# Performance work log

Hardware: AMD Instinct MI355X
Metric: run time of the kernel (lower is better)

The kernel has to match this reference:

```python
import jax, jax.numpy as jnp
import numpy as np

B, N, C, D = 64, 1024, 128, 64

def setup_inputs() -> dict:
    key = jax.random.key(0)
    ks = jax.random.split(key, 7)
    # kaiming_normal_ on weights (fan_in = C), default zero-ish biases kept as Linear default uniform; use small uniform
    std = float(np.sqrt(2.0 / C))
    bb = float(1.0 / np.sqrt(C))
    return {
        "x": jax.random.normal(ks[0], (B, N, C), jnp.float32),
        "Wq": jax.random.normal(ks[1], (C, D), jnp.float32) * std,
        "bq": jax.random.uniform(ks[2], (D,), jnp.float32, -bb, bb),
        "Wk": jax.random.normal(ks[3], (C, D), jnp.float32) * std,
        "bk": jax.random.uniform(ks[4], (D,), jnp.float32, -bb, bb),
        "Wv": jax.random.normal(ks[5], (C, D), jnp.float32) * std,
        "bv": jax.random.uniform(ks[6], (D,), jnp.float32, -bb, bb),
    }

def reference(x, Wq, bq, Wk, bk, Wv, bv):
    q = jax.nn.relu(jnp.einsum('bnc,cd->bnd', x, Wq) + bq)  # [B,N,D]
    k = jax.nn.relu(jnp.einsum('bnc,cd->bnd', x, Wk) + bk)
    v = jax.nn.relu(jnp.einsum('bnc,cd->bnd', x, Wv) + bv)
    scores = jnp.einsum('bnd,bmd->bnm', q, k) / jnp.sqrt(jnp.asarray(D, q.dtype))
    attn = jax.nn.softmax(scores, axis=-1)
    out = jnp.einsum('bnm,bmd->bnd', attn, v)
    return out + q
```

## Files before the change

### kernel.cpp

```cpp
#include <hip/hip_runtime.h>
#include <hip/hip_bf16.h>


#define Bsz 64
#define Nsz 1024
#define Csz 128
#define Dsz 64

typedef __attribute__((ext_vector_type(8))) short short8;
typedef __attribute__((ext_vector_type(4))) float f32x4;
typedef __attribute__((ext_vector_type(4))) short s16x4;

__device__ __forceinline__ unsigned short f2bf(float f) {
    union { float f; unsigned u; } v; v.f = f;
    unsigned r = v.u + 0x7FFF + ((v.u >> 16) & 1);
    return (unsigned short)(r >> 16);
}
__device__ __forceinline__ float bf2f(unsigned short h) {
    union { unsigned u; float f; } v; v.u = ((unsigned)h) << 16;
    return v.f;
}

__global__ __launch_bounds__(256, 3) void qkv_kernel(
    const float* __restrict__ x,
    const float* __restrict__ Wq, const float* __restrict__ bq,
    const float* __restrict__ Wk, const float* __restrict__ bk,
    const float* __restrict__ Wv, const float* __restrict__ bv,
    float* __restrict__ qf, unsigned short* __restrict__ qs,
    unsigned short* __restrict__ ksc, unsigned short* __restrict__ vt)
{
    __shared__ short xh[8192];
    __shared__ short xl[8192];
    const int t    = threadIdx.x;
    const int lane = t & 63;
    const int l16  = lane & 15, quad = lane >> 4;
    const int dt   = t >> 6;
    const long rowbase = (long)blockIdx.x * 64;

    {
        const int row = t & 63;
        const float* xrow = x + (rowbase + row) * Csz;
        #pragma unroll
        for (int p = 0; p < 4; p++) {
            int cb = (t >> 6) + p * 4;
            float4 a = *(const float4*)(xrow + cb * 8);
            float4 b = *(const float4*)(xrow + cb * 8 + 4);
            float f[8] = {a.x, a.y, a.z, a.w, b.x, b.y, b.z, b.w};
            short8 hi, lo;
            #pragma unroll
            for (int i = 0; i < 8; i++) {
                unsigned short h = f2bf(f[i]);
                hi[i] = (short)h;
                lo[i] = (short)f2bf(f[i] - bf2f(h));
            }
            int unit = ((row >> 4) * 4 + (cb >> 2)) * 64 + ((row & 15) | ((cb & 3) << 4));
            *(short8*)&xh[unit * 8] = hi;
            *(short8*)&xl[unit * 8] = lo;
        }
    }

    short8 wqh[4], wql[4], wkf[4], wvf[4];
    #pragma unroll
    for (int ksi = 0; ksi < 4; ksi++) {
        #pragma unroll
        for (int j = 0; j < 8; j++) {
            int c = ksi * 32 + quad * 8 + j;
            int d = dt * 16 + l16;
            float w = Wq[c * Dsz + d];
            unsigned short h = f2bf(w);
            wqh[ksi][j] = (short)h;
            wql[ksi][j] = (short)f2bf(w - bf2f(h));
            wkf[ksi][j] = (short)f2bf(Wk[c * Dsz + d]);
            wvf[ksi][j] = (short)f2bf(Wv[c * Dsz + d]);
        }
    }
    __syncthreads();

    f32x4 aq[4], akk[4], avv[4];
    #pragma unroll
    for (int i = 0; i < 4; i++) {
        aq[i]  = (f32x4){0.f, 0.f, 0.f, 0.f};
        akk[i] = (f32x4){0.f, 0.f, 0.f, 0.f};
        avv[i] = (f32x4){0.f, 0.f, 0.f, 0.f};
    }

    #pragma unroll
    for (int ksi = 0; ksi < 4; ksi++) {
        #pragma unroll
        for (int rt = 0; rt < 4; rt++) {
            short8 ah = *(const short8*)&xh[((rt * 4 + ksi) * 64 + lane) * 8];
            short8 al = *(const short8*)&xl[((rt * 4 + ksi) * 64 + lane) * 8];
            aq[rt]  = __builtin_amdgcn_mfma_f32_16x16x32_bf16(ah, wqh[ksi], aq[rt], 0, 0, 0);
            aq[rt]  = __builtin_amdgcn_mfma_f32_16x16x32_bf16(al, wqh[ksi], aq[rt], 0, 0, 0);
            aq[rt]  = __builtin_amdgcn_mfma_f32_16x16x32_bf16(ah, wql[ksi], aq[rt], 0, 0, 0);
            akk[rt] = __builtin_amdgcn_mfma_f32_16x16x32_bf16(ah, wkf[ksi], akk[rt], 0, 0, 0);
            avv[rt] = __builtin_amdgcn_mfma_f32_16x16x32_bf16(ah, wvf[ksi], avv[rt], 0, 0, 0);
        }
    }

    const int d = dt * 16 + l16;
    const float bqd = bq[d], bkd = bk[d], bvd = bv[d];
    const long bidx = rowbase >> 10;
    const int nloc = (int)(rowbase & 1023);
    const float SC = 0.125f * 1.44269504f;
    unsigned short* vrow = vt + bidx * (Dsz * Nsz) + (long)d * Nsz + nloc;
    #pragma unroll
    for (int rt = 0; rt < 4; rt++) {
        #pragma unroll
        for (int r = 0; r < 4; r++) {
            long n = rowbase + rt * 16 + quad * 4 + r;
            float q = fmaxf(aq[rt][r]  + bqd, 0.f);
            float k = fmaxf(akk[rt][r] + bkd, 0.f);
            float v = fmaxf(avv[rt][r] + bvd, 0.f);
            qf[n * Dsz + d]  = q;
            qs[n * Dsz + d]  = f2bf(q * SC);
            ksc[n * Dsz + d] = f2bf(k);
            vrow[(quad * 4 + r) * 4 + rt] = f2bf(v);
        }
    }
}

__global__ __launch_bounds__(256) void attn_kernel(
    const unsigned short* __restrict__ qs,
    const unsigned short* __restrict__ ksc,
    const unsigned short* __restrict__ vt,
    const float* __restrict__ qf,
    float* __restrict__ out)
{
    __shared__ short Ks[64][72];
    __shared__ short Vt[64][72];
    __shared__ short Pl[4][16][72];

    const int t    = threadIdx.x;
    const int wave = t >> 6;
    const int lane = t & 63;
    const int l16  = lane & 15;
    const int quad = lane >> 4;
    const int b    = blockIdx.x & 63;
    const int qt   = blockIdx.x >> 6;

    const long qrow = (long)b * Nsz + qt * 64 + wave * 16 + l16;
    const short8 aq0 = *(const short8*)(qs + qrow * Dsz + quad * 8);
    const short8 aq1 = *(const short8*)(qs + qrow * Dsz + 32 + quad * 8);

    f32x4 O[4];
    #pragma unroll
    for (int cb = 0; cb < 4; cb++) O[cb] = (f32x4){0.f, 0.f, 0.f, 0.f};
    float lsum[4] = {0.f, 0.f, 0.f, 0.f};

    const unsigned short* kbatch = ksc + (long)b * Nsz * Dsz;
    const unsigned short* vbatch = vt  + (long)b * Dsz * Nsz;

    for (int kt = 0; kt < 16; kt++) {
        const unsigned short* kg = kbatch + (long)kt * 64 * Dsz;
        #pragma unroll
        for (int p = 0; p < 2; p++) {
            int idx = t + p * 256;
            int key = idx >> 3, dc = (idx & 7) * 8;
            *(short8*)&Ks[key][dc] = *(const short8*)(kg + key * Dsz + dc);
        }
        const unsigned short* vg = vbatch + kt * 64;
        #pragma unroll
        for (int p = 0; p < 2; p++) {
            int idx = t + p * 256;
            int dim = idx >> 3, kc = (idx & 7) * 8;
            *(short8*)&Vt[dim][kc] = *(const short8*)(vg + (long)dim * Nsz + kc);
        }
        __syncthreads();

        f32x4 s[4];
        #pragma unroll
        for (int kb = 0; kb < 4; kb++) {
            short8 b0 = *(const short8*)&Ks[kb * 16 + l16][quad * 8];
            short8 b1 = *(const short8*)&Ks[kb * 16 + l16][32 + quad * 8];
            f32x4 acc = (f32x4){0.f, 0.f, 0.f, 0.f};
            acc = __builtin_amdgcn_mfma_f32_16x16x32_bf16(aq0, b0, acc, 0, 0, 0);
            acc = __builtin_amdgcn_mfma_f32_16x16x32_bf16(aq1, b1, acc, 0, 0, 0);
            s[kb] = acc;
        }

        #pragma unroll
        for (int r = 0; r < 4; r++) {
            float p0 = __builtin_amdgcn_exp2f(s[0][r]);
            float p1 = __builtin_amdgcn_exp2f(s[1][r]);
            float p2 = __builtin_amdgcn_exp2f(s[2][r]);
            float p3 = __builtin_amdgcn_exp2f(s[3][r]);
            lsum[r] += (p0 + p1) + (p2 + p3);
            s16x4 pk = { (short)f2bf(p0), (short)f2bf(p1),
                         (short)f2bf(p2), (short)f2bf(p3) };
            *(s16x4*)&Pl[wave][quad * 4 + r][l16 * 4] = pk;
        }

        #pragma unroll
        for (int ck = 0; ck < 2; ck++) {
            short8 ap = *(const short8*)&Pl[wave][l16][ck * 32 + quad * 8];
            #pragma unroll
            for (int cb = 0; cb < 4; cb++) {
                short8 bv = *(const short8*)&Vt[cb * 16 + l16][ck * 32 + quad * 8];
                O[cb] = __builtin_amdgcn_mfma_f32_16x16x32_bf16(ap, bv, O[cb], 0, 0, 0);
            }
        }
        __syncthreads();
    }

    #pragma unroll
    for (int r = 0; r < 4; r++) {
        #pragma unroll
        for (int off = 1; off < 16; off <<= 1)
            lsum[r] += __shfl_xor(lsum[r], off);
    }

    const long obase = ((long)b * Nsz + qt * 64 + wave * 16) * Dsz;
    #pragma unroll
    for (int r = 0; r < 4; r++) {
        float rl = 1.0f / lsum[r];
        int row = quad * 4 + r;
        #pragma unroll
        for (int cb = 0; cb < 4; cb++) {
            long idx = obase + (long)row * Dsz + cb * 16 + l16;
            out[idx] = O[cb][r] * rl + qf[idx];
        }
    }
}

extern "C" void kernel_launch(void* const* d_in, const int* in_sizes, int n_in,
                              void* d_out, int out_size, void* d_ws, size_t ws_size,
                              hipStream_t stream) {
    const float* x  = (const float*)d_in[0];
    const float* Wq = (const float*)d_in[1];
    const float* bq = (const float*)d_in[2];
    const float* Wk = (const float*)d_in[3];
    const float* bk = (const float*)d_in[4];
    const float* Wv = (const float*)d_in[5];
    const float* bv = (const float*)d_in[6];
    float* out = (float*)d_out;

    char* ws = (char*)d_ws;
    float*          qf  = (float*)ws;
    unsigned short* qsc = (unsigned short*)(ws + 16777216);
    unsigned short* ksc = (unsigned short*)(ws + 25165824);
    unsigned short* vtc = (unsigned short*)(ws + 33554432);

    qkv_kernel<<<dim3(1024), dim3(256), 0, stream>>>(
        x, Wq, bq, Wk, bk, Wv, bv, qf, qsc, ksc, vtc);
    attn_kernel<<<dim3(Bsz * 16), dim3(256), 0, stream>>>(
        qsc, ksc, vtc, qf, out);
}
```

Baseline: 144.0 us.

## Drop fp32 Q buffer, load K/V directly to registers, double query rows per wave

```diff
diff --git a/kernel.cpp b/kernel.cpp
--- a/kernel.cpp
+++ b/kernel.cpp
@@ -9,7 +9,6 @@
 
 typedef __attribute__((ext_vector_type(8))) short short8;
 typedef __attribute__((ext_vector_type(4))) float f32x4;
-typedef __attribute__((ext_vector_type(4))) short s16x4;
 
 __device__ __forceinline__ unsigned short f2bf(float f) {
     union { float f; unsigned u; } v; v.f = f;
@@ -20,14 +19,22 @@
     union { unsigned u; float f; } v; v.u = ((unsigned)h) << 16;
     return v.f;
 }
-
-__global__ __launch_bounds__(256, 3) void qkv_kernel(
+__device__ __forceinline__ unsigned pack_bf16rn(float lo, float hi) {
+    unsigned ulo = __float_as_uint(lo) + 0x8000u;
+    unsigned uhi = __float_as_uint(hi) + 0x8000u;
+    return __builtin_amdgcn_perm(uhi, ulo, 0x07060302u);
+}
+
+#define SCq (0.125f * 1.44269504f)
+#define INV_SC (1.0f / (0.125f * 1.44269504f))
+
+__global__ __launch_bounds__(256, 2) void qkv_kernel(
     const float* __restrict__ x,
     const float* __restrict__ Wq, const float* __restrict__ bq,
     const float* __restrict__ Wk, const float* __restrict__ bk,
     const float* __restrict__ Wv, const float* __restrict__ bv,
-    float* __restrict__ qf, unsigned short* __restrict__ qs,
-    unsigned short* __restrict__ ksc, unsigned short* __restrict__ vt)
+    unsigned short* __restrict__ qs, unsigned short* __restrict__ ksc,
+    unsigned short* __restrict__ vt)
 {
     __shared__ short xh[8192];
     __shared__ short xl[8192];
@@ -35,29 +42,8 @@
     const int lane = t & 63;
     const int l16  = lane & 15, quad = lane >> 4;
     const int dt   = t >> 6;
-    const long rowbase = (long)blockIdx.x * 64;
-
-    {
-        const int row = t & 63;
-        const float* xrow = x + (rowbase + row) * Csz;
-        #pragma unroll
-        for (int p = 0; p < 4; p++) {
-            int cb = (t >> 6) + p * 4;
-            float4 a = *(const float4*)(xrow + cb * 8);
-            float4 b = *(const float4*)(xrow + cb * 8 + 4);
-            float f[8] = {a.x, a.y, a.z, a.w, b.x, b.y, b.z, b.w};
-            short8 hi, lo;
-            #pragma unroll
-            for (int i = 0; i < 8; i++) {
-                unsigned short h = f2bf(f[i]);
-                hi[i] = (short)h;
-                lo[i] = (short)f2bf(f[i] - bf2f(h));
-            }
-            int unit = ((row >> 4) * 4 + (cb >> 2)) * 64 + ((row & 15) | ((cb & 3) << 4));
-            *(short8*)&xh[unit * 8] = hi;
-            *(short8*)&xl[unit * 8] = lo;
-        }
-    }
+    const long rowbase = (long)blockIdx.x * 128;
+    const int d = dt * 16 + l16;
 
     short8 wqh[4], wql[4], wkf[4], wvf[4];
     #pragma unroll
@@ -65,7 +51,6 @@
         #pragma unroll
         for (int j = 0; j < 8; j++) {
             int c = ksi * 32 + quad * 8 + j;
-            int d = dt * 16 + l16;
             float w = Wq[c * Dsz + d];
             unsigned short h = f2bf(w);
             wqh[ksi][j] = (short)h;
@@ -74,62 +59,88 @@
             wvf[ksi][j] = (short)f2bf(Wv[c * Dsz + d]);
         }
     }
-    __syncthreads();
-
-    f32x4 aq[4], akk[4], avv[4];
-    #pragma unroll
-    for (int i = 0; i < 4; i++) {
-        aq[i]  = (f32x4){0.f, 0.f, 0.f, 0.f};
-        akk[i] = (f32x4){0.f, 0.f, 0.f, 0.f};
-        avv[i] = (f32x4){0.f, 0.f, 0.f, 0.f};
-    }
-
-    #pragma unroll
-    for (int ksi = 0; ksi < 4; ksi++) {
+    const float bqd = bq[d], bkd = bk[d], bvd = bv[d];
+    const long b = rowbase >> 10;
+
+    for (int chunk = 0; chunk < 2; chunk++) {
+        const long rowc = rowbase + chunk * 64;
+        if (chunk) __syncthreads();
+
+        {
+            const int row = t & 63;
+            const float* xrow = x + (rowc + row) * Csz;
+            #pragma unroll
+            for (int p = 0; p < 4; p++) {
+                int cb = (t >> 6) + p * 4;
+                float4 a = *(const float4*)(xrow + cb * 8);
+                float4 bb = *(const float4*)(xrow + cb * 8 + 4);
+                float f[8] = {a.x, a.y, a.z, a.w, bb.x, bb.y, bb.z, bb.w};
+                short8 hi, lo;
+                #pragma unroll
+                for (int i = 0; i < 8; i++) {
+                    unsigned short h = f2bf(f[i]);
+                    hi[i] = (short)h;
+                    lo[i] = (short)f2bf(f[i] - bf2f(h));
+                }
+                int unit = ((row >> 4) * 4 + (cb >> 2)) * 64 + ((row & 15) | ((cb & 3) << 4));
+                *(short8*)&xh[unit * 8] = hi;
+                *(short8*)&xl[unit * 8] = lo;
+            }
+        }
+        __syncthreads();
+
+        f32x4 aq[4], ak[4], av[4];
+        #pragma unroll
+        for (int i = 0; i < 4; i++) {
+            aq[i] = (f32x4){0.f, 0.f, 0.f, 0.f};
+            ak[i] = (f32x4){0.f, 0.f, 0.f, 0.f};
+            av[i] = (f32x4){0.f, 0.f, 0.f, 0.f};
+        }
+        #pragma unroll
+        for (int ksi = 0; ksi < 4; ksi++) {
+            #pragma unroll
+            for (int rt = 0; rt < 4; rt++) {
+                short8 ah = *(const short8*)&xh[((rt * 4 + ksi) * 64 + lane) * 8];
+                short8 al = *(const short8*)&xl[((rt * 4 + ksi) * 64 + lane) * 8];
+                aq[rt] = __builtin_amdgcn_mfma_f32_16x16x32_bf16(ah, wqh[ksi], aq[rt], 0, 0, 0);
+                aq[rt] = __builtin_amdgcn_mfma_f32_16x16x32_bf16(al, wqh[ksi], aq[rt], 0, 0, 0);
+                aq[rt] = __builtin_amdgcn_mfma_f32_16x16x32_bf16(ah, wql[ksi], aq[rt], 0, 0, 0);
+                ak[rt] = __builtin_amdgcn_mfma_f32_16x16x32_bf16(ah, wkf[ksi], ak[rt], 0, 0, 0);
+                av[rt] = __builtin_amdgcn_mfma_f32_16x16x32_bf16(ah, wvf[ksi], av[rt], 0, 0, 0);
+            }
+        }
+
+        float vv[16];
         #pragma unroll
         for (int rt = 0; rt < 4; rt++) {
-            short8 ah = *(const short8*)&xh[((rt * 4 + ksi) * 64 + lane) * 8];
-            short8 al = *(const short8*)&xl[((rt * 4 + ksi) * 64 + lane) * 8];
-            aq[rt]  = __builtin_amdgcn_mfma_f32_16x16x32_bf16(ah, wqh[ksi], aq[rt], 0, 0, 0);
-            aq[rt]  = __builtin_amdgcn_mfma_f32_16x16x32_bf16(al, wqh[ksi], aq[rt], 0, 0, 0);
-            aq[rt]  = __builtin_amdgcn_mfma_f32_16x16x32_bf16(ah, wql[ksi], aq[rt], 0, 0, 0);
-            akk[rt] = __builtin_amdgcn_mfma_f32_16x16x32_bf16(ah, wkf[ksi], akk[rt], 0, 0, 0);
-            avv[rt] = __builtin_amdgcn_mfma_f32_16x16x32_bf16(ah, wvf[ksi], avv[rt], 0, 0, 0);
-        }
-    }
-
-    const int d = dt * 16 + l16;
-    const float bqd = bq[d], bkd = bk[d], bvd = bv[d];
-    const long bidx = rowbase >> 10;
-    const int nloc = (int)(rowbase & 1023);
-    const float SC = 0.125f * 1.44269504f;
-    unsigned short* vrow = vt + bidx * (Dsz * Nsz) + (long)d * Nsz + nloc;
-    #pragma unroll
-    for (int rt = 0; rt < 4; rt++) {
-        #pragma unroll
-        for (int r = 0; r < 4; r++) {
-            long n = rowbase + rt * 16 + quad * 4 + r;
-            float q = fmaxf(aq[rt][r]  + bqd, 0.f);
-            float k = fmaxf(akk[rt][r] + bkd, 0.f);
-            float v = fmaxf(avv[rt][r] + bvd, 0.f);
-            qf[n * Dsz + d]  = q;
-            qs[n * Dsz + d]  = f2bf(q * SC);
-            ksc[n * Dsz + d] = f2bf(k);
-            vrow[(quad * 4 + r) * 4 + rt] = f2bf(v);
-        }
-    }
-}
-
-__global__ __launch_bounds__(256) void attn_kernel(
+            #pragma unroll
+            for (int r = 0; r < 4; r++) {
+                long n = rowc + rt * 16 + quad * 4 + r;
+                float q = fmaxf(aq[rt][r] + bqd, 0.f);
+                float k = fmaxf(ak[rt][r] + bkd, 0.f);
+                float v = fmaxf(av[rt][r] + bvd, 0.f);
+                qs[n * Dsz + d]  = f2bf(q * SCq);
+                ksc[n * Dsz + d] = f2bf(k);
+                vv[r * 4 + rt] = v;
+            }
+        }
+        unsigned short* vp = vt + b * (Dsz * Nsz) + (long)d * Nsz + (rowc & 1023) + quad * 16;
+        uint4 p0 = make_uint4(pack_bf16rn(vv[0], vv[1]),  pack_bf16rn(vv[2], vv[3]),
+                              pack_bf16rn(vv[4], vv[5]),  pack_bf16rn(vv[6], vv[7]));
+        uint4 p1 = make_uint4(pack_bf16rn(vv[8], vv[9]),  pack_bf16rn(vv[10], vv[11]),
+                              pack_bf16rn(vv[12], vv[13]), pack_bf16rn(vv[14], vv[15]));
+        *(uint4*)vp = p0;
+        *(uint4*)(vp + 8) = p1;
+    }
+}
+
+__global__ __launch_bounds__(256, 2) void attn_kernel(
     const unsigned short* __restrict__ qs,
     const unsigned short* __restrict__ ksc,
     const unsigned short* __restrict__ vt,
-    const float* __restrict__ qf,
     float* __restrict__ out)
 {
-    __shared__ short Ks[64][72];
-    __shared__ short Vt[64][72];
-    __shared__ short Pl[4][16][72];
+    __shared__ short Pl[4][32][72];
 
     const int t    = threadIdx.x;
     const int wave = t >> 6;
@@ -137,88 +148,119 @@
     const int l16  = lane & 15;
     const int quad = lane >> 4;
     const int b    = blockIdx.x & 63;
-    const int qt   = blockIdx.x >> 6;
-
-    const long qrow = (long)b * Nsz + qt * 64 + wave * 16 + l16;
-    const short8 aq0 = *(const short8*)(qs + qrow * Dsz + quad * 8);
-    const short8 aq1 = *(const short8*)(qs + qrow * Dsz + 32 + quad * 8);
-
-    f32x4 O[4];
-    #pragma unroll
-    for (int cb = 0; cb < 4; cb++) O[cb] = (f32x4){0.f, 0.f, 0.f, 0.f};
-    float lsum[4] = {0.f, 0.f, 0.f, 0.f};
-
-    const unsigned short* kbatch = ksc + (long)b * Nsz * Dsz;
-    const unsigned short* vbatch = vt  + (long)b * Dsz * Nsz;
+    const int qh   = blockIdx.x >> 6;
+    const int qbase = qh * 128 + wave * 32;
+
+    const unsigned short* kb_ = ksc + (long)b * (Nsz * Dsz);
+    const unsigned short* vb_ = vt  + (long)b * (Dsz * Nsz);
+
+    short8 aq[2][2];
+    #pragma unroll
+    for (int s = 0; s < 2; s++) {
+        const unsigned short* qp = qs + ((long)b * Nsz + qbase + s * 16 + l16) * Dsz + quad * 8;
+        aq[s][0] = *(const short8*)(qp);
+        aq[s][1] = *(const short8*)(qp + 32);
+    }
+
+    f32x4 O[2][4];
+    float lsum[2][4];
+    #pragma unroll
+    for (int s = 0; s < 2; s++) {
+        #pragma unroll
+        for (int i = 0; i < 4; i++) { O[s][i] = (f32x4){0.f, 0.f, 0.f, 0.f}; lsum[s][i] = 0.f; }
+    }
+
+    short8 kf[4][2];
+    #pragma unroll
+    for (int kb = 0; kb < 4; kb++) {
+        const unsigned short* p = kb_ + (long)(kb * 16 + l16) * Dsz + quad * 8;
+        kf[kb][0] = *(const short8*)(p);
+        kf[kb][1] = *(const short8*)(p + 32);
+    }
 
     for (int kt = 0; kt < 16; kt++) {
-        const unsigned short* kg = kbatch + (long)kt * 64 * Dsz;
-        #pragma unroll
-        for (int p = 0; p < 2; p++) {
-            int idx = t + p * 256;
-            int key = idx >> 3, dc = (idx & 7) * 8;
-            *(short8*)&Ks[key][dc] = *(const short8*)(kg + key * Dsz + dc);
-        }
-        const unsigned short* vg = vbatch + kt * 64;
-        #pragma unroll
-        for (int p = 0; p < 2; p++) {
-            int idx = t + p * 256;
-            int dim = idx >> 3, kc = (idx & 7) * 8;
-            *(short8*)&Vt[dim][kc] = *(const short8*)(vg + (long)dim * Nsz + kc);
-        }
-        __syncthreads();
-
-        f32x4 s[4];
-        #pragma unroll
-        for (int kb = 0; kb < 4; kb++) {
-            short8 b0 = *(const short8*)&Ks[kb * 16 + l16][quad * 8];
-            short8 b1 = *(const short8*)&Ks[kb * 16 + l16][32 + quad * 8];
-            f32x4 acc = (f32x4){0.f, 0.f, 0.f, 0.f};
-            acc = __builtin_amdgcn_mfma_f32_16x16x32_bf16(aq0, b0, acc, 0, 0, 0);
-            acc = __builtin_amdgcn_mfma_f32_16x16x32_bf16(aq1, b1, acc, 0, 0, 0);
-            s[kb] = acc;
-        }
-
+        short8 bvf[2][4];
+        #pragma unroll
+        for (int ck = 0; ck < 2; ck++) {
+            #pragma unroll
+            for (int cb = 0; cb < 4; cb++) {
+                bvf[ck][cb] = *(const short8*)(vb_ + (long)(cb * 16 + l16) * Nsz
+                                               + kt * 64 + ck * 32 + quad * 8);
+            }
+        }
+
+        #pragma unroll
+        for (int s = 0; s < 2; s++) {
+            f32x4 sc[4];
+            #pragma unroll
+            for (int kb = 0; kb < 4; kb++) {
+                f32x4 z = (f32x4){0.f, 0.f, 0.f, 0.f};
+                z = __builtin_amdgcn_mfma_f32_16x16x32_bf16(aq[s][0], kf[kb][0], z, 0, 0, 0);
+                z = __builtin_amdgcn_mfma_f32_16x16x32_bf16(aq[s][1], kf[kb][1], z, 0, 0, 0);
+                sc[kb] = z;
+            }
+            #pragma unroll
+            for (int r = 0; r < 4; r++) {
+                float p0 = __builtin_amdgcn_exp2f(sc[0][r]);
+                float p1 = __builtin_amdgcn_exp2f(sc[1][r]);
+                float p2 = __builtin_amdgcn_exp2f(sc[2][r]);
+                float p3 = __builtin_amdgcn_exp2f(sc[3][r]);
+                lsum[s][r] += (p0 + p1) + (p2 + p3);
+                unsigned pk01 = pack_bf16rn(p0, p1);
+                unsigned pk23 = pack_bf16rn(p2, p3);
+                *(uint2*)&Pl[wave][s * 16 + quad * 4 + r][l16 * 4] = make_uint2(pk01, pk23);
+            }
+        }
+
+        short8 kf2[4][2];
+        {
+            int ktn = (kt + 1) & 15;
+            #pragma unroll
+            for (int kb = 0; kb < 4; kb++) {
+                const unsigned short* p = kb_ + (long)(ktn * 64 + kb * 16 + l16) * Dsz + quad * 8;
+                kf2[kb][0] = *(const short8*)(p);
+                kf2[kb][1] = *(const short8*)(p + 32);
+            }
+        }
+
+        #pragma unroll
+        for (int ck = 0; ck < 2; ck++) {
+            #pragma unroll
+            for (int s = 0; s < 2; s++) {
+                short8 ap = *(const short8*)&Pl[wave][s * 16 + l16][ck * 32 + quad * 8];
+                #pragma unroll
+                for (int cb = 0; cb < 4; cb++) {
+                    O[s][cb] = __builtin_amdgcn_mfma_f32_16x16x32_bf16(ap, bvf[ck][cb], O[s][cb], 0, 0, 0);
+                }
+            }
+        }
+
+        #pragma unroll
+        for (int kb = 0; kb < 4; kb++) { kf[kb][0] = kf2[kb][0]; kf[kb][1] = kf2[kb][1]; }
+    }
+
+    #pragma unroll
+    for (int s = 0; s < 2; s++) {
         #pragma unroll
         for (int r = 0; r < 4; r++) {
-            float p0 = __builtin_amdgcn_exp2f(s[0][r]);
-            float p1 = __builtin_amdgcn_exp2f(s[1][r]);
-            float p2 = __builtin_amdgcn_exp2f(s[2][r]);
-            float p3 = __builtin_amdgcn_exp2f(s[3][r]);
-            lsum[r] += (p0 + p1) + (p2 + p3);
-            s16x4 pk = { (short)f2bf(p0), (short)f2bf(p1),
-                         (short)f2bf(p2), (short)f2bf(p3) };
-            *(s16x4*)&Pl[wave][quad * 4 + r][l16 * 4] = pk;
-        }
-
-        #pragma unroll
-        for (int ck = 0; ck < 2; ck++) {
-            short8 ap = *(const short8*)&Pl[wave][l16][ck * 32 + quad * 8];
+            #pragma unroll
+            for (int off = 1; off < 16; off <<= 1)
+                lsum[s][r] += __shfl_xor(lsum[s][r], off);
+        }
+    }
+
+    #pragma unroll
+    for (int s = 0; s < 2; s++) {
+        #pragma unroll
+        for (int r = 0; r < 4; r++) {
+            float rl = 1.0f / lsum[s][r];
+            long nrow = (long)b * Nsz + qbase + s * 16 + quad * 4 + r;
             #pragma unroll
             for (int cb = 0; cb < 4; cb++) {
-                short8 bv = *(const short8*)&Vt[cb * 16 + l16][ck * 32 + quad * 8];
-                O[cb] = __builtin_amdgcn_mfma_f32_16x16x32_bf16(ap, bv, O[cb], 0, 0, 0);
-            }
-        }
-        __syncthreads();
-    }
-
-    #pragma unroll
-    for (int r = 0; r < 4; r++) {
-        #pragma unroll
-        for (int off = 1; off < 16; off <<= 1)
-            lsum[r] += __shfl_xor(lsum[r], off);
-    }
-
-    const long obase = ((long)b * Nsz + qt * 64 + wave * 16) * Dsz;
-    #pragma unroll
-    for (int r = 0; r < 4; r++) {
-        float rl = 1.0f / lsum[r];
-        int row = quad * 4 + r;
-        #pragma unroll
-        for (int cb = 0; cb < 4; cb++) {
-            long idx = obase + (long)row * Dsz + cb * 16 + l16;
-            out[idx] = O[cb][r] * rl + qf[idx];
+                int d = cb * 16 + l16;
+                float qv = bf2f(qs[nrow * Dsz + d]) * INV_SC;
+                out[nrow * Dsz + d] = O[s][cb][r] * rl + qv;
+            }
         }
     }
 }
@@ -236,13 +278,12 @@
     float* out = (float*)d_out;
 
     char* ws = (char*)d_ws;
-    float*          qf  = (float*)ws;
-    unsigned short* qsc = (unsigned short*)(ws + 16777216);
-    unsigned short* ksc = (unsigned short*)(ws + 25165824);
-    unsigned short* vtc = (unsigned short*)(ws + 33554432);
-
-    qkv_kernel<<<dim3(1024), dim3(256), 0, stream>>>(
-        x, Wq, bq, Wk, bk, Wv, bv, qf, qsc, ksc, vtc);
-    attn_kernel<<<dim3(Bsz * 16), dim3(256), 0, stream>>>(
-        qsc, ksc, vtc, qf, out);
-}
+    unsigned short* qsc = (unsigned short*)ws;
+    unsigned short* ksc = (unsigned short*)(ws + 0x1000000);
+    unsigned short* vtc = (unsigned short*)(ws + 0x2000000);
+
+    qkv_kernel<<<dim3(512), dim3(256), 0, stream>>>(
+        x, Wq, bq, Wk, bk, Wv, bv, qsc, ksc, vtc);
+    attn_kernel<<<dim3(512), dim3(256), 0, stream>>>(
+        qsc, ksc, vtc, out);
+}
```

Result: slower. 160.1 us (+11.2%).
